# Kernel tuning notes

Measured on AMD Instinct MI355X. Metric: run time of the kernel, lower is better.

Reference implementation:

```python
import jax, jax.numpy as jnp
import numpy as np

B, Q, K = 4, 128, 1024
DQ, DK, DV, H = 512, 512, 512, 256
NEG_INF = -1e6


def setup_inputs() -> dict:
    key = jax.random.key(0)
    ks = jax.random.split(key, 6)
    queries = jax.random.normal(ks[0], (B, Q, DQ), dtype=jnp.float32)
    keys = jax.random.normal(ks[1], (B, K, DK), dtype=jnp.float32)
    values = jax.random.normal(ks[2], (B, K, DV), dtype=jnp.float32)
    valid_lens = jax.random.randint(ks[3], (B,), 1, K + 1, dtype=jnp.int32)
    # Learned params (Dense use_bias=False): W_q [DQ,H], W_k [DK,H], w_v [H] (Dense(1) squeezed)
    Wq = jax.random.normal(ks[4], (DQ, H), dtype=jnp.float32) / np.sqrt(DQ)
    Wk = jax.random.normal(ks[5], (DK, H), dtype=jnp.float32) / np.sqrt(DK)
    wv = jax.random.normal(jax.random.fold_in(key, 7), (H,), dtype=jnp.float32) / np.sqrt(H)
    return {"queries": queries, "keys": keys, "values": values,
            "valid_lens": valid_lens, "Wq": Wq, "Wk": Wk, "wv": wv}


def reference(queries, keys, values, valid_lens, Wq, Wk, wv):
    q = queries @ Wq                       # [B,Q,H]
    k = keys @ Wk                          # [B,K,H]
    feats = jnp.tanh(q[:, :, None, :] + k[:, None, :, :])   # [B,Q,K,H]
    scores = jnp.einsum('bqkh,h->bqk', feats, wv)            # [B,Q,K]
    mask = jnp.arange(scores.shape[-1]) < valid_lens[:, None, None]  # [B,1,K]
    scores = jnp.where(mask, scores, NEG_INF)
    attn = jax.nn.softmax(scores, axis=-1)                   # [B,Q,K]
    # dropout is identity at inference
    return attn @ values                                     # [B,Q,DV]
```

## Files before the change

kernel.cpp:

```cpp
#include <hip/hip_runtime.h>

#define Bn 4
#define Qn 128
#define Kn 1024
#define Dn 512
#define Hn 256

__device__ __forceinline__ float fast_tanh(float x) {
    float e = __expf(2.0f * x);
    return 1.0f - 2.0f * __builtin_amdgcn_rcpf(1.0f + e);
}

#define PBK 64

__global__ __launch_bounds__(256) void proj_kernel(
    const float* __restrict__ queries, const float* __restrict__ keys,
    const float* __restrict__ Wq, const float* __restrict__ Wk,
    const int* __restrict__ valid_lens,
    float* __restrict__ qproj, float* __restrict__ kproj)
{
    const int blk = blockIdx.x;
    const int nt = blk & 3;
    const int mt = blk >> 2;
    const int t = threadIdx.x;
    const float* Asrc; const float* W; float* Dst;
    int m0;
    if (mt < 8) {
        m0 = mt * 64;
        Asrc = queries; W = Wq; Dst = qproj;
    } else {
        int r0 = (mt - 8) * 64;
        int b = r0 >> 10;
        if ((r0 & 1023) >= valid_lens[b]) return;
        m0 = r0;
        Asrc = keys; W = Wk; Dst = kproj;
    }
    const int n0 = nt * 64;

    __shared__ float s_a[PBK][68];
    __shared__ float s_b[PBK][64];

    const int trow = t >> 4;
    const int tcol = t & 15;

    float acc[4][4] = {{0.f}};
    float4 ra[4], rb[4];

    #pragma unroll
    for (int i = 0; i < 4; ++i) {
        int row = (t >> 4) + i * 16, c4 = t & 15;
        ra[i] = *(const float4*)(Asrc + (size_t)(m0 + row) * Dn + c4 * 4);
        rb[i] = *(const float4*)(W + (size_t)row * Hn + n0 + c4 * 4);
    }

    for (int kt = 0; kt < 8; ++kt) {
        __syncthreads();
        #pragma unroll
        for (int i = 0; i < 4; ++i) {
            int row = (t >> 4) + i * 16, c4 = t & 15;
            s_a[c4 * 4 + 0][row] = ra[i].x;
            s_a[c4 * 4 + 1][row] = ra[i].y;
            s_a[c4 * 4 + 2][row] = ra[i].z;
            s_a[c4 * 4 + 3][row] = ra[i].w;
            *(float4*)&s_b[row][c4 * 4] = rb[i];
        }
        __syncthreads();
        if (kt < 7) {
            const int d0n = (kt + 1) * PBK;
            #pragma unroll
            for (int i = 0; i < 4; ++i) {
                int row = (t >> 4) + i * 16, c4 = t & 15;
                ra[i] = *(const float4*)(Asrc + (size_t)(m0 + row) * Dn + d0n + c4 * 4);
                rb[i] = *(const float4*)(W + (size_t)(d0n + row) * Hn + n0 + c4 * 4);
            }
        }
        #pragma unroll 16
        for (int kk = 0; kk < PBK; ++kk) {
            float4 a4 = *(const float4*)&s_a[kk][trow * 4];
            float4 b4 = *(const float4*)&s_b[kk][tcol * 4];
            float a[4] = {a4.x, a4.y, a4.z, a4.w};
            float b[4] = {b4.x, b4.y, b4.z, b4.w};
            #pragma unroll
            for (int i = 0; i < 4; ++i)
                #pragma unroll
                for (int j = 0; j < 4; ++j)
                    acc[i][j] += a[i] * b[j];
        }
    }
    #pragma unroll
    for (int i = 0; i < 4; ++i) {
        float4 o; o.x = acc[i][0]; o.y = acc[i][1]; o.z = acc[i][2]; o.w = acc[i][3];
        *(float4*)(Dst + (size_t)(m0 + trow * 4 + i) * Hn + n0 + tcol * 4) = o;
    }
}

#define SK_KT 16
#define SK_PAD 260

__global__ __launch_bounds__(256) void score_kernel(
    const float* __restrict__ qproj, const float* __restrict__ kproj,
    const float* __restrict__ wv, const int* __restrict__ valid_lens,
    float* __restrict__ escores, float* __restrict__ rowsum)
{
    const int blk = blockIdx.x;
    const int kt = blk & 63;
    const int qt = (blk >> 6) & 31;
    const int b  = blk >> 11;
    const int vlen = valid_lens[b];
    const int k0 = kt * SK_KT;
    if (k0 >= vlen) return;
    const int q0 = qt * 4;
    const int t = threadIdx.x;

    __shared__ float s_k[SK_KT * SK_PAD];
    __shared__ float s_q[4 * Hn];
    __shared__ float s_wv[Hn];

    {
        const float4* src = reinterpret_cast<const float4*>(
            kproj + ((size_t)b * Kn + k0) * Hn);
        #pragma unroll
        for (int i = 0; i < 4; ++i) {
            int idx = t + i * 256;
            int row = idx >> 6, c4 = idx & 63;
            *reinterpret_cast<float4*>(&s_k[row * SK_PAD + c4 * 4]) = src[idx];
        }
        reinterpret_cast<float4*>(s_q)[t] = reinterpret_cast<const float4*>(
            qproj + ((size_t)b * Qn + q0) * Hn)[t];
        if (t < 64)
            reinterpret_cast<float4*>(s_wv)[t] =
                reinterpret_cast<const float4*>(wv)[t];
    }
    __syncthreads();

    const int wave = t >> 6;
    const int lane = t & 63;
    const int kloc = lane & 15;
    const int hq   = lane >> 4;

    const float4* kr = reinterpret_cast<const float4*>(&s_k[kloc * SK_PAD + hq * 64]);
    const float4* qr = reinterpret_cast<const float4*>(&s_q[wave * Hn + hq * 64]);
    const float4* wr = reinterpret_cast<const float4*>(&s_wv[hq * 64]);

    float s = 0.0f;
    #pragma unroll
    for (int i = 0; i < 16; ++i) {
        float4 kv = kr[i];
        float4 qv = qr[i];
        float4 wq = wr[i];
        s += wq.x * fast_tanh(qv.x + kv.x);
        s += wq.y * fast_tanh(qv.y + kv.y);
        s += wq.z * fast_tanh(qv.z + kv.z);
        s += wq.w * fast_tanh(qv.w + kv.w);
    }
    s += __shfl_xor(s, 16, 64);
    s += __shfl_xor(s, 32, 64);

    const int k = k0 + kloc;
    float e = 0.0f;
    if (lane < 16 && k < vlen) {
        e = __expf(s);
        escores[((size_t)b * Qn + q0 + wave) * Kn + k] = e;
    }
    #pragma unroll
    for (int off = 32; off; off >>= 1)
        e += __shfl_xor(e, off, 64);
    if (lane == 0)
        atomicAdd(&rowsum[b * Qn + q0 + wave], e);
}

__global__ __launch_bounds__(256) void av_part_kernel(
    const float* __restrict__ escores, const float* __restrict__ values,
    float* __restrict__ parts)
{
    const int blk = blockIdx.x;
    const int kc = blk & 3;
    const int dh = (blk >> 2) & 1;
    const int qt = (blk >> 3) & 15;
    const int b  = blk >> 7;
    const int t = threadIdx.x;
    const int q0 = qt * 8;
    const int kb = kc * 256;
    const int d  = dh * 256 + t;

    __shared__ float s_e[8][256];
    #pragma unroll
    for (int i = 0; i < 2; ++i) {
        int idx = t + i * 256;
        int row = idx >> 6, c4 = idx & 63;
        *(float4*)&s_e[row][c4 * 4] = *(const float4*)(
            escores + ((size_t)(b * Qn + q0 + row)) * Kn + kb + c4 * 4);
    }
    __syncthreads();

    const float* vb = values + ((size_t)b * Kn + kb) * Dn + d;
    float acc[8] = {0.f};
    #pragma unroll 2
    for (int k = 0; k < 256; k += 4) {
        float v0 = vb[(size_t)(k + 0) * Dn];
        float v1 = vb[(size_t)(k + 1) * Dn];
        float v2 = vb[(size_t)(k + 2) * Dn];
        float v3 = vb[(size_t)(k + 3) * Dn];
        #pragma unroll
        for (int j = 0; j < 8; ++j) {
            float4 e4 = *(const float4*)&s_e[j][k];
            acc[j] += e4.x * v0 + e4.y * v1 + e4.z * v2 + e4.w * v3;
        }
    }
    float* pp = parts + (size_t)kc * (Bn * Qn * Dn)
                      + ((size_t)(b * Qn + q0)) * Dn + d;
    #pragma unroll
    for (int j = 0; j < 8; ++j)
        pp[(size_t)j * Dn] = acc[j];
}

__global__ __launch_bounds__(256) void reduce_kernel(
    const float* __restrict__ parts, const float* __restrict__ rowsum,
    float* __restrict__ out)
{
    const int idx = blockIdx.x * 256 + threadIdx.x;
    const int row = (idx * 4) >> 9;
    const float inv = __builtin_amdgcn_rcpf(rowsum[row]);
    const float4* p = (const float4*)parts;
    float4 a = p[idx];
    float4 b = p[idx + 65536];
    float4 c = p[idx + 131072];
    float4 d = p[idx + 196608];
    float4 o;
    o.x = (a.x + b.x + c.x + d.x) * inv;
    o.y = (a.y + b.y + c.y + d.y) * inv;
    o.z = (a.z + b.z + c.z + d.z) * inv;
    o.w = (a.w + b.w + c.w + d.w) * inv;
    ((float4*)out)[idx] = o;
}

extern "C" void kernel_launch(void* const* d_in, const int* in_sizes, int n_in,
                              void* d_out, int out_size, void* d_ws, size_t ws_size,
                              hipStream_t stream) {
    const float* queries    = (const float*)d_in[0];
    const float* keys       = (const float*)d_in[1];
    const float* values     = (const float*)d_in[2];
    const int*   valid_lens = (const int*)  d_in[3];
    const float* Wq         = (const float*)d_in[4];
    const float* Wk         = (const float*)d_in[5];
    const float* wv         = (const float*)d_in[6];
    float* out = (float*)d_out;

    float* qproj   = (float*)d_ws;
    float* kproj   = qproj + Bn * Qn * Hn;
    float* escores = kproj + Bn * Kn * Hn;
    float* rowsum  = escores + Bn * Qn * Kn;
    float* parts   = kproj;

    hipMemsetAsync(escores, 0, (size_t)(Bn * Qn * Kn + Bn * Qn) * sizeof(float),
                   stream);
    proj_kernel<<<288, 256, 0, stream>>>(queries, keys, Wq, Wk, valid_lens,
                                         qproj, kproj);
    score_kernel<<<Bn * 32 * 64, 256, 0, stream>>>(qproj, kproj, wv,
                                                   valid_lens, escores, rowsum);
    av_part_kernel<<<512, 256, 0, stream>>>(escores, values, parts);
    reduce_kernel<<<256, 256, 0, stream>>>(parts, rowsum, out);
}
```

Baseline: 169.2 us.

## Split projection GEMM inner K loop across two thread halves with smem reduction

The projection kernel now launches 512 threads per block, and each half of the block accumulates half of each 64-wide K tile. Global loads are spread across all 512 threads, and the two partial 4x4 accumulators are summed through shared memory before the store. The aim is more parallelism and latency hiding for a grid of only 288 blocks, at the cost of an extra reduction pass and extra barriers.

Result: faster. 157.1 us (-7.2%).

```diff
diff --git a/kernel.cpp b/kernel.cpp
--- a/kernel.cpp
+++ b/kernel.cpp
@@ -13,7 +13,7 @@
 
 #define PBK 64
 
-__global__ __launch_bounds__(256) void proj_kernel(
+__global__ __launch_bounds__(512, 4) void proj_kernel(
     const float* __restrict__ queries, const float* __restrict__ keys,
     const float* __restrict__ Wq, const float* __restrict__ Wk,
     const int* __restrict__ valid_lens,
@@ -40,44 +40,48 @@
     __shared__ float s_a[PBK][68];
     __shared__ float s_b[PBK][64];
 
-    const int trow = t >> 4;
-    const int tcol = t & 15;
+    const int tt   = t & 255;
+    const int kh   = t >> 8;
+    const int trow = tt >> 4;
+    const int tcol = tt & 15;
+    const int kklo = kh << 5;
+
+    const int lrow = t >> 4;
+    const int lc4  = t & 15;
 
     float acc[4][4] = {{0.f}};
-    float4 ra[4], rb[4];
-
-    #pragma unroll
-    for (int i = 0; i < 4; ++i) {
-        int row = (t >> 4) + i * 16, c4 = t & 15;
-        ra[i] = *(const float4*)(Asrc + (size_t)(m0 + row) * Dn + c4 * 4);
-        rb[i] = *(const float4*)(W + (size_t)row * Hn + n0 + c4 * 4);
+    float4 ra[2], rb[2];
+
+    #pragma unroll
+    for (int i = 0; i < 2; ++i) {
+        ra[i] = *(const float4*)(Asrc + (size_t)(m0 + lrow + i * 32) * Dn + lc4 * 4);
+        rb[i] = *(const float4*)(W + (size_t)(lrow + i * 32) * Hn + n0 + lc4 * 4);
     }
 
     for (int kt = 0; kt < 8; ++kt) {
         __syncthreads();
         #pragma unroll
-        for (int i = 0; i < 4; ++i) {
-            int row = (t >> 4) + i * 16, c4 = t & 15;
-            s_a[c4 * 4 + 0][row] = ra[i].x;
-            s_a[c4 * 4 + 1][row] = ra[i].y;
-            s_a[c4 * 4 + 2][row] = ra[i].z;
-            s_a[c4 * 4 + 3][row] = ra[i].w;
-            *(float4*)&s_b[row][c4 * 4] = rb[i];
+        for (int i = 0; i < 2; ++i) {
+            int row = lrow + i * 32;
+            s_a[lc4 * 4 + 0][row] = ra[i].x;
+            s_a[lc4 * 4 + 1][row] = ra[i].y;
+            s_a[lc4 * 4 + 2][row] = ra[i].z;
+            s_a[lc4 * 4 + 3][row] = ra[i].w;
+            *(float4*)&s_b[row][lc4 * 4] = rb[i];
         }
         __syncthreads();
         if (kt < 7) {
             const int d0n = (kt + 1) * PBK;
             #pragma unroll
-            for (int i = 0; i < 4; ++i) {
-                int row = (t >> 4) + i * 16, c4 = t & 15;
-                ra[i] = *(const float4*)(Asrc + (size_t)(m0 + row) * Dn + d0n + c4 * 4);
-                rb[i] = *(const float4*)(W + (size_t)(d0n + row) * Hn + n0 + c4 * 4);
+            for (int i = 0; i < 2; ++i) {
+                ra[i] = *(const float4*)(Asrc + (size_t)(m0 + lrow + i * 32) * Dn + d0n + lc4 * 4);
+                rb[i] = *(const float4*)(W + (size_t)(d0n + lrow + i * 32) * Hn + n0 + lc4 * 4);
             }
         }
-        #pragma unroll 16
-        for (int kk = 0; kk < PBK; ++kk) {
-            float4 a4 = *(const float4*)&s_a[kk][trow * 4];
-            float4 b4 = *(const float4*)&s_b[kk][tcol * 4];
+        #pragma unroll
+        for (int kk = 0; kk < 32; ++kk) {
+            float4 a4 = *(const float4*)&s_a[kklo + kk][trow * 4];
+            float4 b4 = *(const float4*)&s_b[kklo + kk][tcol * 4];
             float a[4] = {a4.x, a4.y, a4.z, a4.w};
             float b[4] = {b4.x, b4.y, b4.z, b4.w};
             #pragma unroll
@@ -87,10 +91,27 @@
                     acc[i][j] += a[i] * b[j];
         }
     }
-    #pragma unroll
-    for (int i = 0; i < 4; ++i) {
-        float4 o; o.x = acc[i][0]; o.y = acc[i][1]; o.z = acc[i][2]; o.w = acc[i][3];
-        *(float4*)(Dst + (size_t)(m0 + trow * 4 + i) * Hn + n0 + tcol * 4) = o;
+
+    __syncthreads();
+    float* red = &s_a[0][0];
+    if (kh) {
+        #pragma unroll
+        for (int i = 0; i < 4; ++i)
+            #pragma unroll
+            for (int j = 0; j < 4; ++j)
+                red[tt * 17 + i * 4 + j] = acc[i][j];
+    }
+    __syncthreads();
+    if (!kh) {
+        #pragma unroll
+        for (int i = 0; i < 4; ++i) {
+            float4 o;
+            o.x = acc[i][0] + red[tt * 17 + i * 4 + 0];
+            o.y = acc[i][1] + red[tt * 17 + i * 4 + 1];
+            o.z = acc[i][2] + red[tt * 17 + i * 4 + 2];
+            o.w = acc[i][3] + red[tt * 17 + i * 4 + 3];
+            *(float4*)(Dst + (size_t)(m0 + trow * 4 + i) * Hn + n0 + tcol * 4) = o;
+        }
     }
 }
 
@@ -254,7 +275,7 @@
 
     hipMemsetAsync(escores, 0, (size_t)(Bn * Qn * Kn + Bn * Qn) * sizeof(float),
                    stream);
-    proj_kernel<<<288, 256, 0, stream>>>(queries, keys, Wq, Wk, valid_lens,
+    proj_kernel<<<288, 512, 0, stream>>>(queries, keys, Wq, Wk, valid_lens,
                                          qproj, kproj);
     score_kernel<<<Bn * 32 * 64, 256, 0, stream>>>(qproj, kproj, wv,
                                                    valid_lens, escores, rowsum);
```
